# Kernel tuning notes

Measured on AMD Instinct MI355X. Metric: run time of the kernel, lower is better.

Reference implementation:

```python
import jax, jax.numpy as jnp
import numpy as np

B, S, F, H = 512, 1024, 16, 64
BN_EPS = 1e-3  # Keras BatchNormalization default epsilon


def setup_inputs() -> dict:
    key = jax.random.key(0)
    ks = jax.random.split(key, 8)
    scale = 0.1
    return {
        "inputs": jax.random.normal(ks[0], (B, S, F), dtype=jnp.float32),
        "gru_kernel": jax.random.normal(ks[1], (F - 1, 3 * H), dtype=jnp.float32) * scale,
        "gru_rec_kernel": jax.random.normal(ks[2], (H, 3 * H), dtype=jnp.float32) * scale,
        "gru_bias": jax.random.normal(ks[3], (2, 3 * H), dtype=jnp.float32) * scale,
        "w1": jax.random.normal(ks[4], (H, 64), dtype=jnp.float32) * scale,
        "b1": jnp.zeros((64,), dtype=jnp.float32),
        "bn_gamma": jnp.ones((64,), dtype=jnp.float32),
        "bn_beta": jnp.zeros((64,), dtype=jnp.float32),
        "bn_mean": jnp.zeros((64,), dtype=jnp.float32),
        "bn_var": jnp.ones((64,), dtype=jnp.float32),
        "w2": jax.random.normal(ks[5], (64, 1), dtype=jnp.float32) * scale,
        "b2": jnp.zeros((1,), dtype=jnp.float32),
        "T": jax.random.normal(ks[6], (1,), dtype=jnp.float32),
    }


def _gru_scan(x, kernel, rec_kernel, bias):
    # Keras GRU, reset_after=True, gate order (z, r, h). x: [B, S, Fin]
    b_i, b_r = bias[0], bias[1]  # input bias, recurrent bias, each [3H]
    # Precompute input projections for all timesteps: [B, S, 3H]
    x_proj = jnp.einsum("bsf,fg->bsg", x, kernel) + b_i
    h0 = jnp.zeros((x.shape[0], rec_kernel.shape[0]), dtype=x.dtype)

    def step(h, xp):
        rp = h @ rec_kernel + b_r  # [B, 3H]
        xz, xr, xh = jnp.split(xp, 3, axis=-1)
        rz, rr, rh = jnp.split(rp, 3, axis=-1)
        z = jax.nn.sigmoid(xz + rz)
        r = jax.nn.sigmoid(xr + rr)
        hh = jnp.tanh(xh + r * rh)
        h_new = z * h + (1.0 - z) * hh
        return h_new, None

    h_final, _ = jax.lax.scan(step, h0, jnp.swapaxes(x_proj, 0, 1))
    return h_final  # [B, H]


def reference(inputs, gru_kernel, gru_rec_kernel, gru_bias, w1, b1,
              bn_gamma, bn_beta, bn_mean, bn_var, w2, b2, T):
    x = inputs[:, :, :-1]                 # [B, S, F-1]
    delta_x_shifted = inputs[:, :, -1]    # [B, S]
    state = _gru_scan(x, gru_kernel, gru_rec_kernel, gru_bias)  # [B, H]
    # T * delta tiled to H then mean over time == T * mean_t(delta), broadcast over H
    delta_effect = T[0] * jnp.mean(delta_x_shifted, axis=1, keepdims=True)  # [B, 1]
    state = state + delta_effect  # broadcasts over H
    h = jax.nn.relu(state @ w1 + b1)
    # Dropout identity at inference; BatchNorm uses moving statistics
    h = (h - bn_mean) * jax.lax.rsqrt(bn_var + BN_EPS) * bn_gamma + bn_beta
    out = h @ w2 + b2  # [B, 1]
    return out
```

## Files before the change

kernel.cpp:

```cpp
#include <hip/hip_runtime.h>
#include <hip/hip_bf16.h>


#define KEEP(x) asm volatile("" : "+v"(x))

typedef _Float16 f16x2 __attribute__((ext_vector_type(2)));
union H2U { unsigned int u; f16x2 h; };
union FU  { unsigned int u; float f; };

#if defined(__has_builtin)
#  if __has_builtin(__builtin_amdgcn_fdot2)
#    define HAS_FDOT2 1
#  endif
#endif
#ifndef HAS_FDOT2
#  define HAS_FDOT2 0
#endif

static __device__ __forceinline__ float dot2acc(unsigned int hraw, unsigned int wraw, float acc) {
    H2U a, b; a.u = hraw; b.u = wraw;
#if HAS_FDOT2
    return __builtin_amdgcn_fdot2(a.h, b.h, acc, false);
#else
    return fmaf((float)a.h.x, (float)b.h.x, fmaf((float)a.h.y, (float)b.h.y, acc));
#endif
}

template<bool BF16>
struct IO {
    static __device__ __forceinline__ float ld(const void* p, int i) {
        if constexpr (BF16) {
            unsigned short u = ((const unsigned short*)p)[i];
            FU c; c.u = (unsigned int)u << 16;
            return c.f;
        } else {
            return ((const float*)p)[i];
        }
    }
    static __device__ __forceinline__ void st(void* p, int i, float v) {
        if constexpr (BF16) ((__hip_bfloat16*)p)[i] = __float2bfloat16(v);
        else ((float*)p)[i] = v;
    }
};

__global__ void detect_dtype_kernel(const void* rkbuf, int* flag) {
    const float* f = (const float*)rkbuf;
    int ok = 0;
    for (int i = 0; i < 64; ++i) {
        float a = fabsf(f[i]);
        ok += (a > 1e-5f && a < 2.0f) ? 1 : 0;
    }
    *flag = (ok >= 48) ? 1 : 0;
}

template<bool BF16>
__global__ __launch_bounds__(64, 1)
void gru_sw_kernel(const void* __restrict__ inp, const void* __restrict__ gk,
                   const void* __restrict__ rk,  const void* __restrict__ gb,
                   const void* __restrict__ w1,  const void* __restrict__ b1v,
                   const void* __restrict__ gam, const void* __restrict__ bet,
                   const void* __restrict__ muv, const void* __restrict__ vav,
                   const void* __restrict__ w2,  const void* __restrict__ bb2,
                   const void* __restrict__ Tp,  const int* __restrict__ mode,
                   void* __restrict__ out)
{
    const int want = BF16 ? 0 : 1;
    if (*mode != want) return;

    const int b = blockIdx.x;
    const int l = threadIdx.x;

    __shared__ __align__(16) unsigned char xsm[32768];
    __shared__ __align__(16) _Float16 hsf[64];
    __shared__ __align__(16) float sredf[64];

    using io = IO<BF16>;
    const uint4* gin = (const uint4*)inp;
    uint4* xv = (uint4*)xsm;

    if constexpr (BF16) {
#pragma unroll 4
        for (int i = 0; i < 32; ++i)
            xv[i*64 + l] = gin[b*2048 + i*64 + l];
    } else {
#pragma unroll 4
        for (int i = 0; i < 32; ++i)
            xv[i*64 + l] = gin[b*4096 + i*64 + l];
    }

    unsigned int wzp[32], wrp[32], whp[32];
#pragma unroll
    for (int p = 0; p < 32; ++p) {
        H2U z, r, hh;
        z.h  = f16x2{(_Float16)io::ld(rk, (2*p)*192 + l),
                     (_Float16)io::ld(rk, (2*p+1)*192 + l)};
        r.h  = f16x2{(_Float16)io::ld(rk, (2*p)*192 + 64 + l),
                     (_Float16)io::ld(rk, (2*p+1)*192 + 64 + l)};
        hh.h = f16x2{(_Float16)io::ld(rk, (2*p)*192 + 128 + l),
                     (_Float16)io::ld(rk, (2*p+1)*192 + 128 + l)};
        wzp[p] = z.u; wrp[p] = r.u; whp[p] = hh.u;
        KEEP(wzp[p]); KEEP(wrp[p]); KEEP(whp[p]);
    }
    float kzf[15], krf[15], khf[15];
#pragma unroll
    for (int c = 0; c < 15; ++c) {
        kzf[c] = io::ld(gk, c*192 + l);
        krf[c] = io::ld(gk, c*192 + 64 + l);
        khf[c] = io::ld(gk, c*192 + 128 + l);
        KEEP(kzf[c]); KEEP(krf[c]); KEEP(khf[c]);
    }
    const float bz  = io::ld(gb, l)      + io::ld(gb, 192 + l);
    const float br  = io::ld(gb, 64 + l) + io::ld(gb, 192 + 64 + l);
    const float bax = io::ld(gb, 128 + l);
    const float bah = io::ld(gb, 192 + 128 + l);

    float dsum = 0.0f;
    if constexpr (BF16) {
        const unsigned short* xs16 = (const unsigned short*)xsm;
#pragma unroll
        for (int k = 0; k < 16; ++k) {
            FU c; c.u = (unsigned int)xs16[(l + 64*k)*16 + 15] << 16;
            dsum += c.f;
        }
    } else {
        const float* xsf = (const float*)xsm;
#pragma unroll
        for (int k = 0; k < 8; ++k)
            dsum += xsf[(l + 64*k)*16 + 15];
    }

    uint4 hr[8];
#pragma unroll
    for (int i = 0; i < 8; ++i) hr[i] = make_uint4(0, 0, 0, 0);
    float h = 0.0f;

    uint4  cr16[2] = {}, pr16[2] = {};
    float4 cr32[4] = {}, pr32[4] = {};
    if constexpr (BF16) { cr16[0] = xv[0]; cr16[1] = xv[1]; }
    else { const float4* lp = (const float4*)xsm;
           cr32[0]=lp[0]; cr32[1]=lp[1]; cr32[2]=lp[2]; cr32[3]=lp[3]; }

#pragma unroll 1
    for (int s = 0; s < 1024; ++s) {
        if constexpr (!BF16) {
            if (s == 512) {
#pragma unroll 4
                for (int i = 0; i < 32; ++i)
                    xv[i*64 + l] = gin[b*4096 + 2048 + i*64 + l];
                const float* xsf = (const float*)xsm;
#pragma unroll
                for (int k = 0; k < 8; ++k)
                    dsum += xsf[(l + 64*k)*16 + 15];
                const float4* lp = (const float4*)xsm;
                cr32[0]=lp[0]; cr32[1]=lp[1]; cr32[2]=lp[2]; cr32[3]=lp[3];
            }
        }

        float xc[16];
        if constexpr (BF16) {
            const unsigned int dw[8] = {cr16[0].x, cr16[0].y, cr16[0].z, cr16[0].w,
                                        cr16[1].x, cr16[1].y, cr16[1].z, cr16[1].w};
#pragma unroll
            for (int j = 0; j < 8; ++j) {
                FU lo, hi; lo.u = dw[j] << 16; hi.u = dw[j] & 0xffff0000u;
                xc[2*j] = lo.f; xc[2*j+1] = hi.f;
            }
        } else {
            xc[0]=cr32[0].x; xc[1]=cr32[0].y; xc[2]=cr32[0].z; xc[3]=cr32[0].w;
            xc[4]=cr32[1].x; xc[5]=cr32[1].y; xc[6]=cr32[1].z; xc[7]=cr32[1].w;
            xc[8]=cr32[2].x; xc[9]=cr32[2].y; xc[10]=cr32[2].z; xc[11]=cr32[2].w;
            xc[12]=cr32[3].x; xc[13]=cr32[3].y; xc[14]=cr32[3].z; xc[15]=cr32[3].w;
        }
        float az = bz, ar_ = br, ax = bax;
#pragma unroll
        for (int c = 0; c < 15; ++c) {
            az  = fmaf(xc[c], kzf[c], az);
            ar_ = fmaf(xc[c], krf[c], ar_);
            ax  = fmaf(xc[c], khf[c], ax);
        }

        const bool pf = (s < 1023) && (BF16 || s != 511);
        if (pf) {
            if constexpr (BF16) {
                pr16[0] = xv[(s+1)*2]; pr16[1] = xv[(s+1)*2 + 1];
            } else {
                const float4* lp = (const float4*)xsm;
                pr32[0] = lp[((s+1)&511)*4];     pr32[1] = lp[((s+1)&511)*4+1];
                pr32[2] = lp[((s+1)&511)*4+2];   pr32[3] = lp[((s+1)&511)*4+3];
            }
        }

        float ah = bah;
        float az1 = 0.0f, ar1 = 0.0f, ah1 = 0.0f;
#pragma unroll
        for (int i = 0; i < 4; ++i) {
            const uint4 d = hr[i];
            az  = dot2acc(d.x, wzp[4*i+0], az);  ar_ = dot2acc(d.x, wrp[4*i+0], ar_); ah  = dot2acc(d.x, whp[4*i+0], ah);
            az  = dot2acc(d.y, wzp[4*i+1], az);  ar_ = dot2acc(d.y, wrp[4*i+1], ar_); ah  = dot2acc(d.y, whp[4*i+1], ah);
            az  = dot2acc(d.z, wzp[4*i+2], az);  ar_ = dot2acc(d.z, wrp[4*i+2], ar_); ah  = dot2acc(d.z, whp[4*i+2], ah);
            az  = dot2acc(d.w, wzp[4*i+3], az);  ar_ = dot2acc(d.w, wrp[4*i+3], ar_); ah  = dot2acc(d.w, whp[4*i+3], ah);
        }
#pragma unroll
        for (int i = 4; i < 8; ++i) {
            const uint4 d = hr[i];
            az1 = dot2acc(d.x, wzp[4*i+0], az1); ar1 = dot2acc(d.x, wrp[4*i+0], ar1); ah1 = dot2acc(d.x, whp[4*i+0], ah1);
            az1 = dot2acc(d.y, wzp[4*i+1], az1); ar1 = dot2acc(d.y, wrp[4*i+1], ar1); ah1 = dot2acc(d.y, whp[4*i+1], ah1);
            az1 = dot2acc(d.z, wzp[4*i+2], az1); ar1 = dot2acc(d.z, wrp[4*i+2], ar1); ah1 = dot2acc(d.z, whp[4*i+2], ah1);
            az1 = dot2acc(d.w, wzp[4*i+3], az1); ar1 = dot2acc(d.w, wrp[4*i+3], ar1); ah1 = dot2acc(d.w, whp[4*i+3], ah1);
        }
        az += az1; ar_ += ar1; ah += ah1;

        const float z   = __builtin_amdgcn_rcpf(1.0f + __expf(-az));
        const float r   = __builtin_amdgcn_rcpf(1.0f + __expf(-ar_));
        const float pre = fmaf(r, ah, ax);
        const float e2  = __expf(2.0f * pre);
        const float th  = 1.0f - 2.0f * __builtin_amdgcn_rcpf(e2 + 1.0f);
        h = fmaf(z, h - th, th);

        hsf[l] = (_Float16)h;
        const uint4* hp = (const uint4*)hsf;
#pragma unroll
        for (int i = 0; i < 8; ++i) hr[i] = hp[i];
        if constexpr (BF16) { cr16[0] = pr16[0]; cr16[1] = pr16[1]; }
        else { cr32[0]=pr32[0]; cr32[1]=pr32[1]; cr32[2]=pr32[2]; cr32[3]=pr32[3]; }
    }

#pragma unroll
    for (int off = 1; off < 64; off <<= 1)
        dsum += __shfl_xor(dsum, off, 64);
    const float T0 = io::ld(Tp, 0);
    const float state = fmaf(T0 * (1.0f / 1024.0f), dsum, h);
    sredf[l] = state;

    const int j = l;
    float acc = io::ld(b1v, j);
#pragma unroll
    for (int k = 0; k < 64; ++k)
        acc = fmaf(sredf[k], io::ld(w1, k*64 + j), acc);
    acc = fmaxf(acc, 0.0f);
    const float inv = rsqrtf(io::ld(vav, j) + 0.001f);
    acc = fmaf((acc - io::ld(muv, j)) * inv, io::ld(gam, j), io::ld(bet, j));

    float v = acc * io::ld(w2, j);
#pragma unroll
    for (int off = 32; off > 0; off >>= 1)
        v += __shfl_down(v, off);
    if (j == 0) io::st(out, b, v + io::ld(bb2, 0));
}

extern "C" void kernel_launch(void* const* d_in, const int* in_sizes, int n_in,
                              void* d_out, int out_size, void* d_ws, size_t ws_size,
                              hipStream_t stream)
{
    const void* inp = d_in[0];
    const void* gk  = d_in[1];
    const void* rk  = d_in[2];
    const void* gb  = d_in[3];
    const void* w1  = d_in[4];
    const void* b1v = d_in[5];
    const void* gam = d_in[6];
    const void* bet = d_in[7];
    const void* muv = d_in[8];
    const void* vav = d_in[9];
    const void* w2  = d_in[10];
    const void* bb2 = d_in[11];
    const void* Tp  = d_in[12];

    int* flag = (int*)d_ws;
    detect_dtype_kernel<<<dim3(1), dim3(1), 0, stream>>>(rk, flag);
    gru_sw_kernel<true ><<<dim3(512), dim3(64), 0, stream>>>(
        inp, gk, rk, gb, w1, b1v, gam, bet, muv, vav, w2, bb2, Tp, flag, d_out);
    gru_sw_kernel<false><<<dim3(512), dim3(64), 0, stream>>>(
        inp, gk, rk, gb, w1, b1v, gam, bet, muv, vav, w2, bb2, Tp, flag, d_out);
}
```

Baseline: 554.5 us.

## Move GRU weights from registers to LDS and overlap next-step input projection

Recurrent and input weights are no longer held in per-lane registers. They are staged into shared memory as packed uint4/float4 vectors and streamed through a software-pipelined load inside the step loop. The input projection for step s+1 is now computed after the hidden-state update of step s, which takes it off the critical path at the start of the step. This cuts register pressure but adds about 24 LDS vector loads per step to the serial recurrence. That cost can lengthen each step, since only one wave runs per block.

```diff
diff --git a/kernel.cpp b/kernel.cpp
--- a/kernel.cpp
+++ b/kernel.cpp
@@ -1,8 +1,6 @@
 #include <hip/hip_runtime.h>
 #include <hip/hip_bf16.h>
 
-
-#define KEEP(x) asm volatile("" : "+v"(x))
 
 typedef _Float16 f16x2 __attribute__((ext_vector_type(2)));
 union H2U { unsigned int u; f16x2 h; };
@@ -55,7 +53,7 @@
 
 template<bool BF16>
 __global__ __launch_bounds__(64, 1)
-void gru_sw_kernel(const void* __restrict__ inp, const void* __restrict__ gk,
+void gru_ls_kernel(const void* __restrict__ inp, const void* __restrict__ gk,
                    const void* __restrict__ rk,  const void* __restrict__ gb,
                    const void* __restrict__ w1,  const void* __restrict__ b1v,
                    const void* __restrict__ gam, const void* __restrict__ bet,
@@ -71,44 +69,55 @@
     const int l = threadIdx.x;
 
     __shared__ __align__(16) unsigned char xsm[32768];
+    __shared__ __align__(16) uint4  wvs[8*3*64];
+    __shared__ __align__(16) float4 xws[3*4*64];
     __shared__ __align__(16) _Float16 hsf[64];
     __shared__ __align__(16) float sredf[64];
 
     using io = IO<BF16>;
     const uint4* gin = (const uint4*)inp;
-    uint4* xv = (uint4*)xsm;
+    uint4* xvw = (uint4*)xsm;
 
     if constexpr (BF16) {
 #pragma unroll 4
         for (int i = 0; i < 32; ++i)
-            xv[i*64 + l] = gin[b*2048 + i*64 + l];
+            xvw[i*64 + l] = gin[b*2048 + i*64 + l];
     } else {
 #pragma unroll 4
         for (int i = 0; i < 32; ++i)
-            xv[i*64 + l] = gin[b*4096 + i*64 + l];
-    }
-
-    unsigned int wzp[32], wrp[32], whp[32];
-#pragma unroll
-    for (int p = 0; p < 32; ++p) {
-        H2U z, r, hh;
-        z.h  = f16x2{(_Float16)io::ld(rk, (2*p)*192 + l),
-                     (_Float16)io::ld(rk, (2*p+1)*192 + l)};
-        r.h  = f16x2{(_Float16)io::ld(rk, (2*p)*192 + 64 + l),
-                     (_Float16)io::ld(rk, (2*p+1)*192 + 64 + l)};
-        hh.h = f16x2{(_Float16)io::ld(rk, (2*p)*192 + 128 + l),
-                     (_Float16)io::ld(rk, (2*p+1)*192 + 128 + l)};
-        wzp[p] = z.u; wrp[p] = r.u; whp[p] = hh.u;
-        KEEP(wzp[p]); KEEP(wrp[p]); KEEP(whp[p]);
-    }
-    float kzf[15], krf[15], khf[15];
-#pragma unroll
-    for (int c = 0; c < 15; ++c) {
-        kzf[c] = io::ld(gk, c*192 + l);
-        krf[c] = io::ld(gk, c*192 + 64 + l);
-        khf[c] = io::ld(gk, c*192 + 128 + l);
-        KEEP(kzf[c]); KEEP(krf[c]); KEEP(khf[c]);
-    }
+            xvw[i*64 + l] = gin[b*4096 + i*64 + l];
+    }
+
+#pragma unroll 1
+    for (int i = 0; i < 8; ++i) {
+#pragma unroll
+        for (int g = 0; g < 3; ++g) {
+            unsigned int dw[4];
+#pragma unroll
+            for (int j = 0; j < 4; ++j) {
+                const int p = 4*i + j;
+                H2U u;
+                u.h = f16x2{(_Float16)io::ld(rk, (2*p)*192 + g*64 + l),
+                            (_Float16)io::ld(rk, (2*p+1)*192 + g*64 + l)};
+                dw[j] = u.u;
+            }
+            wvs[(i*3 + g)*64 + l] = make_uint4(dw[0], dw[1], dw[2], dw[3]);
+        }
+    }
+#pragma unroll 1
+    for (int g = 0; g < 3; ++g) {
+#pragma unroll
+        for (int j = 0; j < 4; ++j) {
+            float v[4];
+#pragma unroll
+            for (int c4 = 0; c4 < 4; ++c4) {
+                const int ch = 4*j + c4;
+                v[c4] = (ch < 15) ? io::ld(gk, ch*192 + g*64 + l) : 0.0f;
+            }
+            xws[(g*4 + j)*64 + l] = make_float4(v[0], v[1], v[2], v[3]);
+        }
+    }
+
     const float bz  = io::ld(gb, l)      + io::ld(gb, 192 + l);
     const float br  = io::ld(gb, 64 + l) + io::ld(gb, 192 + 64 + l);
     const float bax = io::ld(gb, 128 + l);
@@ -129,41 +138,24 @@
             dsum += xsf[(l + 64*k)*16 + 15];
     }
 
-    uint4 hr[8];
-#pragma unroll
-    for (int i = 0; i < 8; ++i) hr[i] = make_uint4(0, 0, 0, 0);
-    float h = 0.0f;
-
-    uint4  cr16[2] = {}, pr16[2] = {};
-    float4 cr32[4] = {}, pr32[4] = {};
-    if constexpr (BF16) { cr16[0] = xv[0]; cr16[1] = xv[1]; }
-    else { const float4* lp = (const float4*)xsm;
-           cr32[0]=lp[0]; cr32[1]=lp[1]; cr32[2]=lp[2]; cr32[3]=lp[3]; }
-
-#pragma unroll 1
-    for (int s = 0; s < 1024; ++s) {
-        if constexpr (!BF16) {
-            if (s == 512) {
-#pragma unroll 4
-                for (int i = 0; i < 32; ++i)
-                    xv[i*64 + l] = gin[b*4096 + 2048 + i*64 + l];
-                const float* xsf = (const float*)xsm;
-#pragma unroll
-                for (int k = 0; k < 8; ++k)
-                    dsum += xsf[(l + 64*k)*16 + 15];
-                const float4* lp = (const float4*)xsm;
-                cr32[0]=lp[0]; cr32[1]=lp[1]; cr32[2]=lp[2]; cr32[3]=lp[3];
-            }
-        }
-
+    const uint4*  WVl = wvs + l;
+    const float4* XWl = xws + l;
+    const uint4*  hp  = (const uint4*)hsf;
+    const uint4*  xvr = (const uint4*)xsm;
+
+    uint4  cr16[2] = {};
+    float4 cr32[4] = {};
+
+    float azc, arc, axc;
+    auto xproj = [&]() {
         float xc[16];
         if constexpr (BF16) {
             const unsigned int dw[8] = {cr16[0].x, cr16[0].y, cr16[0].z, cr16[0].w,
                                         cr16[1].x, cr16[1].y, cr16[1].z, cr16[1].w};
 #pragma unroll
-            for (int j = 0; j < 8; ++j) {
-                FU lo, hi; lo.u = dw[j] << 16; hi.u = dw[j] & 0xffff0000u;
-                xc[2*j] = lo.f; xc[2*j+1] = hi.f;
+            for (int j2 = 0; j2 < 8; ++j2) {
+                FU lo, hi; lo.u = dw[j2] << 16; hi.u = dw[j2] & 0xffff0000u;
+                xc[2*j2] = lo.f; xc[2*j2+1] = hi.f;
             }
         } else {
             xc[0]=cr32[0].x; xc[1]=cr32[0].y; xc[2]=cr32[0].z; xc[3]=cr32[0].w;
@@ -171,42 +163,88 @@
             xc[8]=cr32[2].x; xc[9]=cr32[2].y; xc[10]=cr32[2].z; xc[11]=cr32[2].w;
             xc[12]=cr32[3].x; xc[13]=cr32[3].y; xc[14]=cr32[3].z; xc[15]=cr32[3].w;
         }
+        const float4 qz0 = XWl[0],   qz1 = XWl[64],  qz2 = XWl[128], qz3 = XWl[192];
+        const float4 qr0 = XWl[256], qr1 = XWl[320], qr2 = XWl[384], qr3 = XWl[448];
+        const float4 qh0 = XWl[512], qh1 = XWl[576], qh2 = XWl[640], qh3 = XWl[704];
         float az = bz, ar_ = br, ax = bax;
-#pragma unroll
-        for (int c = 0; c < 15; ++c) {
-            az  = fmaf(xc[c], kzf[c], az);
-            ar_ = fmaf(xc[c], krf[c], ar_);
-            ax  = fmaf(xc[c], khf[c], ax);
-        }
-
-        const bool pf = (s < 1023) && (BF16 || s != 511);
-        if (pf) {
+        az=fmaf(xc[0],qz0.x,az);  ar_=fmaf(xc[0],qr0.x,ar_);  ax=fmaf(xc[0],qh0.x,ax);
+        az=fmaf(xc[1],qz0.y,az);  ar_=fmaf(xc[1],qr0.y,ar_);  ax=fmaf(xc[1],qh0.y,ax);
+        az=fmaf(xc[2],qz0.z,az);  ar_=fmaf(xc[2],qr0.z,ar_);  ax=fmaf(xc[2],qh0.z,ax);
+        az=fmaf(xc[3],qz0.w,az);  ar_=fmaf(xc[3],qr0.w,ar_);  ax=fmaf(xc[3],qh0.w,ax);
+        az=fmaf(xc[4],qz1.x,az);  ar_=fmaf(xc[4],qr1.x,ar_);  ax=fmaf(xc[4],qh1.x,ax);
+        az=fmaf(xc[5],qz1.y,az);  ar_=fmaf(xc[5],qr1.y,ar_);  ax=fmaf(xc[5],qh1.y,ax);
+        az=fmaf(xc[6],qz1.z,az);  ar_=fmaf(xc[6],qr1.z,ar_);  ax=fmaf(xc[6],qh1.z,ax);
+        az=fmaf(xc[7],qz1.w,az);  ar_=fmaf(xc[7],qr1.w,ar_);  ax=fmaf(xc[7],qh1.w,ax);
+        az=fmaf(xc[8],qz2.x,az);  ar_=fmaf(xc[8],qr2.x,ar_);  ax=fmaf(xc[8],qh2.x,ax);
+        az=fmaf(xc[9],qz2.y,az);  ar_=fmaf(xc[9],qr2.y,ar_);  ax=fmaf(xc[9],qh2.y,ax);
+        az=fmaf(xc[10],qz2.z,az); ar_=fmaf(xc[10],qr2.z,ar_); ax=fmaf(xc[10],qh2.z,ax);
+        az=fmaf(xc[11],qz2.w,az); ar_=fmaf(xc[11],qr2.w,ar_); ax=fmaf(xc[11],qh2.w,ax);
+        az=fmaf(xc[12],qz3.x,az); ar_=fmaf(xc[12],qr3.x,ar_); ax=fmaf(xc[12],qh3.x,ax);
+        az=fmaf(xc[13],qz3.y,az); ar_=fmaf(xc[13],qr3.y,ar_); ax=fmaf(xc[13],qh3.y,ax);
+        az=fmaf(xc[14],qz3.z,az); ar_=fmaf(xc[14],qr3.z,ar_); ax=fmaf(xc[14],qh3.z,ax);
+        az=fmaf(xc[15],qz3.w,az); ar_=fmaf(xc[15],qr3.w,ar_); ax=fmaf(xc[15],qh3.w,ax);
+        azc = az; arc = ar_; axc = ax;
+    };
+
+    if constexpr (BF16) { cr16[0] = xvr[0]; cr16[1] = xvr[1]; }
+    else { const float4* lp = (const float4*)xsm;
+           cr32[0]=lp[0]; cr32[1]=lp[1]; cr32[2]=lp[2]; cr32[3]=lp[3]; }
+    xproj();
+
+    uint4 hr[8];
+#pragma unroll
+    for (int i = 0; i < 8; ++i) hr[i] = make_uint4(0, 0, 0, 0);
+    float h = 0.0f;
+
+#pragma unroll 1
+    for (int s = 0; s < 1024; ++s) {
+        if constexpr (!BF16) {
+            if (s == 511) {
+#pragma unroll 4
+                for (int i = 0; i < 32; ++i)
+                    xvw[i*64 + l] = gin[b*4096 + 2048 + i*64 + l];
+                const float* xsf = (const float*)xsm;
+#pragma unroll
+                for (int k = 0; k < 8; ++k)
+                    dsum += xsf[(l + 64*k)*16 + 15];
+            }
+        }
+        if (s < 1023) {
             if constexpr (BF16) {
-                pr16[0] = xv[(s+1)*2]; pr16[1] = xv[(s+1)*2 + 1];
+                cr16[0] = xvr[(s+1)*2]; cr16[1] = xvr[(s+1)*2 + 1];
             } else {
                 const float4* lp = (const float4*)xsm;
-                pr32[0] = lp[((s+1)&511)*4];     pr32[1] = lp[((s+1)&511)*4+1];
-                pr32[2] = lp[((s+1)&511)*4+2];   pr32[3] = lp[((s+1)&511)*4+3];
-            }
-        }
-
+                const int ix = ((s+1) & 511) * 4;
+                cr32[0]=lp[ix]; cr32[1]=lp[ix+1]; cr32[2]=lp[ix+2]; cr32[3]=lp[ix+3];
+            }
+        }
+
+        float az = azc, ar_ = arc;
+        const float ax = axc;
         float ah = bah;
         float az1 = 0.0f, ar1 = 0.0f, ah1 = 0.0f;
-#pragma unroll
-        for (int i = 0; i < 4; ++i) {
+        uint4 cz = WVl[0], crr = WVl[64], chh = WVl[128];
+#pragma unroll
+        for (int i = 0; i < 8; ++i) {
+            uint4 nz, nr, nh;
+            if (i < 7) {
+                nz = WVl[(i+1)*192];
+                nr = WVl[(i+1)*192 + 64];
+                nh = WVl[(i+1)*192 + 128];
+            }
             const uint4 d = hr[i];
-            az  = dot2acc(d.x, wzp[4*i+0], az);  ar_ = dot2acc(d.x, wrp[4*i+0], ar_); ah  = dot2acc(d.x, whp[4*i+0], ah);
-            az  = dot2acc(d.y, wzp[4*i+1], az);  ar_ = dot2acc(d.y, wrp[4*i+1], ar_); ah  = dot2acc(d.y, whp[4*i+1], ah);
-            az  = dot2acc(d.z, wzp[4*i+2], az);  ar_ = dot2acc(d.z, wrp[4*i+2], ar_); ah  = dot2acc(d.z, whp[4*i+2], ah);
-            az  = dot2acc(d.w, wzp[4*i+3], az);  ar_ = dot2acc(d.w, wrp[4*i+3], ar_); ah  = dot2acc(d.w, whp[4*i+3], ah);
-        }
-#pragma unroll
-        for (int i = 4; i < 8; ++i) {
-            const uint4 d = hr[i];
-            az1 = dot2acc(d.x, wzp[4*i+0], az1); ar1 = dot2acc(d.x, wrp[4*i+0], ar1); ah1 = dot2acc(d.x, whp[4*i+0], ah1);
-            az1 = dot2acc(d.y, wzp[4*i+1], az1); ar1 = dot2acc(d.y, wrp[4*i+1], ar1); ah1 = dot2acc(d.y, whp[4*i+1], ah1);
-            az1 = dot2acc(d.z, wzp[4*i+2], az1); ar1 = dot2acc(d.z, wrp[4*i+2], ar1); ah1 = dot2acc(d.z, whp[4*i+2], ah1);
-            az1 = dot2acc(d.w, wzp[4*i+3], az1); ar1 = dot2acc(d.w, wrp[4*i+3], ar1); ah1 = dot2acc(d.w, whp[4*i+3], ah1);
+            if (i < 4) {
+                az  = dot2acc(d.x, cz.x, az);  ar_ = dot2acc(d.x, crr.x, ar_); ah  = dot2acc(d.x, chh.x, ah);
+                az  = dot2acc(d.y, cz.y, az);  ar_ = dot2acc(d.y, crr.y, ar_); ah  = dot2acc(d.y, chh.y, ah);
+                az  = dot2acc(d.z, cz.z, az);  ar_ = dot2acc(d.z, crr.z, ar_); ah  = dot2acc(d.z, chh.z, ah);
+                az  = dot2acc(d.w, cz.w, az);  ar_ = dot2acc(d.w, crr.w, ar_); ah  = dot2acc(d.w, chh.w, ah);
+            } else {
+                az1 = dot2acc(d.x, cz.x, az1); ar1 = dot2acc(d.x, crr.x, ar1); ah1 = dot2acc(d.x, chh.x, ah1);
+                az1 = dot2acc(d.y, cz.y, az1); ar1 = dot2acc(d.y, crr.y, ar1); ah1 = dot2acc(d.y, chh.y, ah1);
+                az1 = dot2acc(d.z, cz.z, az1); ar1 = dot2acc(d.z, crr.z, ar1); ah1 = dot2acc(d.z, chh.z, ah1);
+                az1 = dot2acc(d.w, cz.w, az1); ar1 = dot2acc(d.w, crr.w, ar1); ah1 = dot2acc(d.w, chh.w, ah1);
+            }
+            cz = nz; crr = nr; chh = nh;
         }
         az += az1; ar_ += ar1; ah += ah1;
 
@@ -218,11 +256,10 @@
         h = fmaf(z, h - th, th);
 
         hsf[l] = (_Float16)h;
-        const uint4* hp = (const uint4*)hsf;
 #pragma unroll
         for (int i = 0; i < 8; ++i) hr[i] = hp[i];
-        if constexpr (BF16) { cr16[0] = pr16[0]; cr16[1] = pr16[1]; }
-        else { cr32[0]=pr32[0]; cr32[1]=pr32[1]; cr32[2]=pr32[2]; cr32[3]=pr32[3]; }
+
+        if (s < 1023) xproj();
     }
 
 #pragma unroll
@@ -268,8 +305,8 @@
 
     int* flag = (int*)d_ws;
     detect_dtype_kernel<<<dim3(1), dim3(1), 0, stream>>>(rk, flag);
-    gru_sw_kernel<true ><<<dim3(512), dim3(64), 0, stream>>>(
+    gru_ls_kernel<true ><<<dim3(512), dim3(64), 0, stream>>>(
         inp, gk, rk, gb, w1, b1v, gam, bet, muv, vav, w2, bb2, Tp, flag, d_out);
-    gru_sw_kernel<false><<<dim3(512), dim3(64), 0, stream>>>(
+    gru_ls_kernel<false><<<dim3(512), dim3(64), 0, stream>>>(
         inp, gk, rk, gb, w1, b1v, gam, bet, muv, vav, w2, bb2, Tp, flag, d_out);
 }
```

After: 508.5 us. 1.09x faster.

## Pack input projection to fp16 dot2 with LDS-staged weights and split gate chains

Applied to the files above, without the earlier changes.

Replaces the per-step fp32 FMA input projection with packed fp16 dot2 operations. The input-kernel weights are staged in LDS as packed halves and reloaded each step, which frees about 45 VGPRs of fp32 weights. The recurrent matvec is reordered so z is computed first, then r, then h, letting the sigmoid transcendentals overlap the later dot chains. The fp32 second-half refill moves to step 511 and the next-x prefetch moves after the h computation, at the cost of fp16 rounding of the inputs and their weights.

```diff
diff --git a/kernel.cpp b/kernel.cpp
--- a/kernel.cpp
+++ b/kernel.cpp
@@ -17,13 +17,20 @@
 #  define HAS_FDOT2 0
 #endif
 
-static __device__ __forceinline__ float dot2acc(unsigned int hraw, unsigned int wraw, float acc) {
-    H2U a, b; a.u = hraw; b.u = wraw;
+static __device__ __forceinline__ float dot2acc(unsigned int araw, unsigned int braw, float acc) {
+    H2U a, b; a.u = araw; b.u = braw;
 #if HAS_FDOT2
     return __builtin_amdgcn_fdot2(a.h, b.h, acc, false);
 #else
     return fmaf((float)a.h.x, (float)b.h.x, fmaf((float)a.h.y, (float)b.h.y, acc));
 #endif
+}
+
+static __device__ __forceinline__ unsigned int pk16(float lo, float hi) {
+    auto v = __builtin_amdgcn_cvt_pkrtz(lo, hi);
+    union { decltype(v) h; unsigned int u; } u;
+    u.h = v;
+    return u.u;
 }
 
 template<bool BF16>
@@ -55,7 +62,7 @@
 
 template<bool BF16>
 __global__ __launch_bounds__(64, 1)
-void gru_sw_kernel(const void* __restrict__ inp, const void* __restrict__ gk,
+void gru_sx_kernel(const void* __restrict__ inp, const void* __restrict__ gk,
                    const void* __restrict__ rk,  const void* __restrict__ gb,
                    const void* __restrict__ w1,  const void* __restrict__ b1v,
                    const void* __restrict__ gam, const void* __restrict__ bet,
@@ -71,21 +78,39 @@
     const int l = threadIdx.x;
 
     __shared__ __align__(16) unsigned char xsm[32768];
+    __shared__ __align__(16) uint4 xws4[6*64];
     __shared__ __align__(16) _Float16 hsf[64];
     __shared__ __align__(16) float sredf[64];
 
     using io = IO<BF16>;
     const uint4* gin = (const uint4*)inp;
-    uint4* xv = (uint4*)xsm;
+    uint4* xvw = (uint4*)xsm;
 
     if constexpr (BF16) {
 #pragma unroll 4
         for (int i = 0; i < 32; ++i)
-            xv[i*64 + l] = gin[b*2048 + i*64 + l];
+            xvw[i*64 + l] = gin[b*2048 + i*64 + l];
     } else {
 #pragma unroll 4
         for (int i = 0; i < 32; ++i)
-            xv[i*64 + l] = gin[b*4096 + i*64 + l];
+            xvw[i*64 + l] = gin[b*4096 + i*64 + l];
+    }
+
+#pragma unroll 1
+    for (int g = 0; g < 3; ++g) {
+#pragma unroll
+        for (int q = 0; q < 2; ++q) {
+            unsigned int d[4];
+#pragma unroll
+            for (int j = 0; j < 4; ++j) {
+                const int pj = q*4 + j;
+                const int c0 = 2*pj, c1 = 2*pj + 1;
+                const float f0 = (c0 < 15) ? io::ld(gk, c0*192 + g*64 + l) : 0.0f;
+                const float f1 = (c1 < 15) ? io::ld(gk, c1*192 + g*64 + l) : 0.0f;
+                d[j] = pk16(f0, f1);
+            }
+            xws4[(g*2 + q)*64 + l] = make_uint4(d[0], d[1], d[2], d[3]);
+        }
     }
 
     unsigned int wzp[32], wrp[32], whp[32];
@@ -101,14 +126,6 @@
         wzp[p] = z.u; wrp[p] = r.u; whp[p] = hh.u;
         KEEP(wzp[p]); KEEP(wrp[p]); KEEP(whp[p]);
     }
-    float kzf[15], krf[15], khf[15];
-#pragma unroll
-    for (int c = 0; c < 15; ++c) {
-        kzf[c] = io::ld(gk, c*192 + l);
-        krf[c] = io::ld(gk, c*192 + 64 + l);
-        khf[c] = io::ld(gk, c*192 + 128 + l);
-        KEEP(kzf[c]); KEEP(krf[c]); KEEP(khf[c]);
-    }
     const float bz  = io::ld(gb, l)      + io::ld(gb, 192 + l);
     const float br  = io::ld(gb, 64 + l) + io::ld(gb, 192 + 64 + l);
     const float bax = io::ld(gb, 128 + l);
@@ -129,98 +146,158 @@
             dsum += xsf[(l + 64*k)*16 + 15];
     }
 
+    const uint4* hp  = (const uint4*)hsf;
+    const uint4* xvr = (const uint4*)xsm;
+
+    uint4  cr16[2] = {}, pr16[2] = {};
+    float4 cr32[4] = {}, pr32[4] = {};
+    if constexpr (BF16) { cr16[0] = xvr[0]; cr16[1] = xvr[1]; }
+    else { const float4* lp = (const float4*)xsm;
+           cr32[0]=lp[0]; cr32[1]=lp[1]; cr32[2]=lp[2]; cr32[3]=lp[3]; }
+
+    uint4 xwq0, xwq1, xwq2, xwq3, xwq4, xwq5;
+    {
+        const uint4* xq = xws4 + l;
+        xwq0 = xq[0];   xwq1 = xq[64];  xwq2 = xq[128];
+        xwq3 = xq[192]; xwq4 = xq[256]; xwq5 = xq[320];
+    }
+
     uint4 hr[8];
 #pragma unroll
     for (int i = 0; i < 8; ++i) hr[i] = make_uint4(0, 0, 0, 0);
     float h = 0.0f;
-
-    uint4  cr16[2] = {}, pr16[2] = {};
-    float4 cr32[4] = {}, pr32[4] = {};
-    if constexpr (BF16) { cr16[0] = xv[0]; cr16[1] = xv[1]; }
-    else { const float4* lp = (const float4*)xsm;
-           cr32[0]=lp[0]; cr32[1]=lp[1]; cr32[2]=lp[2]; cr32[3]=lp[3]; }
 
 #pragma unroll 1
     for (int s = 0; s < 1024; ++s) {
         if constexpr (!BF16) {
-            if (s == 512) {
+            if (s == 511) {
 #pragma unroll 4
                 for (int i = 0; i < 32; ++i)
-                    xv[i*64 + l] = gin[b*4096 + 2048 + i*64 + l];
+                    xvw[i*64 + l] = gin[b*4096 + 2048 + i*64 + l];
                 const float* xsf = (const float*)xsm;
 #pragma unroll
                 for (int k = 0; k < 8; ++k)
                     dsum += xsf[(l + 64*k)*16 + 15];
-                const float4* lp = (const float4*)xsm;
-                cr32[0]=lp[0]; cr32[1]=lp[1]; cr32[2]=lp[2]; cr32[3]=lp[3];
             }
         }
 
-        float xc[16];
+        unsigned int xcp[8];
         if constexpr (BF16) {
             const unsigned int dw[8] = {cr16[0].x, cr16[0].y, cr16[0].z, cr16[0].w,
                                         cr16[1].x, cr16[1].y, cr16[1].z, cr16[1].w};
 #pragma unroll
             for (int j = 0; j < 8; ++j) {
                 FU lo, hi; lo.u = dw[j] << 16; hi.u = dw[j] & 0xffff0000u;
-                xc[2*j] = lo.f; xc[2*j+1] = hi.f;
+                xcp[j] = pk16(lo.f, hi.f);
             }
         } else {
-            xc[0]=cr32[0].x; xc[1]=cr32[0].y; xc[2]=cr32[0].z; xc[3]=cr32[0].w;
-            xc[4]=cr32[1].x; xc[5]=cr32[1].y; xc[6]=cr32[1].z; xc[7]=cr32[1].w;
-            xc[8]=cr32[2].x; xc[9]=cr32[2].y; xc[10]=cr32[2].z; xc[11]=cr32[2].w;
-            xc[12]=cr32[3].x; xc[13]=cr32[3].y; xc[14]=cr32[3].z; xc[15]=cr32[3].w;
-        }
-        float az = bz, ar_ = br, ax = bax;
-#pragma unroll
-        for (int c = 0; c < 15; ++c) {
-            az  = fmaf(xc[c], kzf[c], az);
-            ar_ = fmaf(xc[c], krf[c], ar_);
-            ax  = fmaf(xc[c], khf[c], ax);
-        }
-
-        const bool pf = (s < 1023) && (BF16 || s != 511);
-        if (pf) {
-            if constexpr (BF16) {
-                pr16[0] = xv[(s+1)*2]; pr16[1] = xv[(s+1)*2 + 1];
-            } else {
-                const float4* lp = (const float4*)xsm;
-                pr32[0] = lp[((s+1)&511)*4];     pr32[1] = lp[((s+1)&511)*4+1];
-                pr32[2] = lp[((s+1)&511)*4+2];   pr32[3] = lp[((s+1)&511)*4+3];
-            }
-        }
-
-        float ah = bah;
-        float az1 = 0.0f, ar1 = 0.0f, ah1 = 0.0f;
+            const float xf[16] = {cr32[0].x,cr32[0].y,cr32[0].z,cr32[0].w,
+                                  cr32[1].x,cr32[1].y,cr32[1].z,cr32[1].w,
+                                  cr32[2].x,cr32[2].y,cr32[2].z,cr32[2].w,
+                                  cr32[3].x,cr32[3].y,cr32[3].z,cr32[3].w};
+#pragma unroll
+            for (int j = 0; j < 8; ++j) xcp[j] = pk16(xf[2*j], xf[2*j+1]);
+        }
+
+        float az = bz, arr = br, ax = bax;
+        {
+            const unsigned int wzx[8] = {xwq0.x,xwq0.y,xwq0.z,xwq0.w, xwq1.x,xwq1.y,xwq1.z,xwq1.w};
+            const unsigned int wrx[8] = {xwq2.x,xwq2.y,xwq2.z,xwq2.w, xwq3.x,xwq3.y,xwq3.z,xwq3.w};
+            const unsigned int whx[8] = {xwq4.x,xwq4.y,xwq4.z,xwq4.w, xwq5.x,xwq5.y,xwq5.z,xwq5.w};
+#pragma unroll
+            for (int j = 0; j < 8; ++j) az  = dot2acc(xcp[j], wzx[j], az);
+#pragma unroll
+            for (int j = 0; j < 8; ++j) arr = dot2acc(xcp[j], wrx[j], arr);
+#pragma unroll
+            for (int j = 0; j < 8; ++j) ax  = dot2acc(xcp[j], whx[j], ax);
+        }
+
+        {
+            unsigned int zz;
+            asm volatile("s_mov_b32 %0, 0" : "=s"(zz));
+            const uint4* xq = xws4 + l + zz;
+            xwq0 = xq[0];   xwq1 = xq[64];  xwq2 = xq[128];
+            xwq3 = xq[192]; xwq4 = xq[256]; xwq5 = xq[320];
+        }
+
+        float az1 = 0.0f;
 #pragma unroll
         for (int i = 0; i < 4; ++i) {
             const uint4 d = hr[i];
-            az  = dot2acc(d.x, wzp[4*i+0], az);  ar_ = dot2acc(d.x, wrp[4*i+0], ar_); ah  = dot2acc(d.x, whp[4*i+0], ah);
-            az  = dot2acc(d.y, wzp[4*i+1], az);  ar_ = dot2acc(d.y, wrp[4*i+1], ar_); ah  = dot2acc(d.y, whp[4*i+1], ah);
-            az  = dot2acc(d.z, wzp[4*i+2], az);  ar_ = dot2acc(d.z, wrp[4*i+2], ar_); ah  = dot2acc(d.z, whp[4*i+2], ah);
-            az  = dot2acc(d.w, wzp[4*i+3], az);  ar_ = dot2acc(d.w, wrp[4*i+3], ar_); ah  = dot2acc(d.w, whp[4*i+3], ah);
+            az  = dot2acc(d.x, wzp[4*i+0], az);
+            az  = dot2acc(d.y, wzp[4*i+1], az);
+            az  = dot2acc(d.z, wzp[4*i+2], az);
+            az  = dot2acc(d.w, wzp[4*i+3], az);
         }
 #pragma unroll
         for (int i = 4; i < 8; ++i) {
             const uint4 d = hr[i];
-            az1 = dot2acc(d.x, wzp[4*i+0], az1); ar1 = dot2acc(d.x, wrp[4*i+0], ar1); ah1 = dot2acc(d.x, whp[4*i+0], ah1);
-            az1 = dot2acc(d.y, wzp[4*i+1], az1); ar1 = dot2acc(d.y, wrp[4*i+1], ar1); ah1 = dot2acc(d.y, whp[4*i+1], ah1);
-            az1 = dot2acc(d.z, wzp[4*i+2], az1); ar1 = dot2acc(d.z, wrp[4*i+2], ar1); ah1 = dot2acc(d.z, whp[4*i+2], ah1);
-            az1 = dot2acc(d.w, wzp[4*i+3], az1); ar1 = dot2acc(d.w, wrp[4*i+3], ar1); ah1 = dot2acc(d.w, whp[4*i+3], ah1);
-        }
-        az += az1; ar_ += ar1; ah += ah1;
-
-        const float z   = __builtin_amdgcn_rcpf(1.0f + __expf(-az));
-        const float r   = __builtin_amdgcn_rcpf(1.0f + __expf(-ar_));
+            az1 = dot2acc(d.x, wzp[4*i+0], az1);
+            az1 = dot2acc(d.y, wzp[4*i+1], az1);
+            az1 = dot2acc(d.z, wzp[4*i+2], az1);
+            az1 = dot2acc(d.w, wzp[4*i+3], az1);
+        }
+        az += az1;
+        const float z = __builtin_amdgcn_rcpf(1.0f + __expf(-az));
+
+        float ar1 = 0.0f;
+#pragma unroll
+        for (int i = 0; i < 4; ++i) {
+            const uint4 d = hr[i];
+            arr = dot2acc(d.x, wrp[4*i+0], arr);
+            arr = dot2acc(d.y, wrp[4*i+1], arr);
+            arr = dot2acc(d.z, wrp[4*i+2], arr);
+            arr = dot2acc(d.w, wrp[4*i+3], arr);
+        }
+#pragma unroll
+        for (int i = 4; i < 8; ++i) {
+            const uint4 d = hr[i];
+            ar1 = dot2acc(d.x, wrp[4*i+0], ar1);
+            ar1 = dot2acc(d.y, wrp[4*i+1], ar1);
+            ar1 = dot2acc(d.z, wrp[4*i+2], ar1);
+            ar1 = dot2acc(d.w, wrp[4*i+3], ar1);
+        }
+        arr += ar1;
+        const float r = __builtin_amdgcn_rcpf(1.0f + __expf(-arr));
+
+        float ah = bah, ah1 = 0.0f;
+#pragma unroll
+        for (int i = 0; i < 4; ++i) {
+            const uint4 d = hr[i];
+            ah  = dot2acc(d.x, whp[4*i+0], ah);
+            ah  = dot2acc(d.y, whp[4*i+1], ah);
+            ah  = dot2acc(d.z, whp[4*i+2], ah);
+            ah  = dot2acc(d.w, whp[4*i+3], ah);
+        }
+#pragma unroll
+        for (int i = 4; i < 8; ++i) {
+            const uint4 d = hr[i];
+            ah1 = dot2acc(d.x, whp[4*i+0], ah1);
+            ah1 = dot2acc(d.y, whp[4*i+1], ah1);
+            ah1 = dot2acc(d.z, whp[4*i+2], ah1);
+            ah1 = dot2acc(d.w, whp[4*i+3], ah1);
+        }
+        ah += ah1;
+
         const float pre = fmaf(r, ah, ax);
         const float e2  = __expf(2.0f * pre);
         const float th  = 1.0f - 2.0f * __builtin_amdgcn_rcpf(e2 + 1.0f);
         h = fmaf(z, h - th, th);
 
+        if (s < 1023) {
+            if constexpr (BF16) {
+                pr16[0] = xvr[(s+1)*2]; pr16[1] = xvr[(s+1)*2 + 1];
+            } else {
+                const float4* lp = (const float4*)xsm;
+                const int ix = ((s+1) & 511) * 4;
+                pr32[0]=lp[ix]; pr32[1]=lp[ix+1]; pr32[2]=lp[ix+2]; pr32[3]=lp[ix+3];
+            }
+        }
+
         hsf[l] = (_Float16)h;
-        const uint4* hp = (const uint4*)hsf;
 #pragma unroll
         for (int i = 0; i < 8; ++i) hr[i] = hp[i];
+
         if constexpr (BF16) { cr16[0] = pr16[0]; cr16[1] = pr16[1]; }
         else { cr32[0]=pr32[0]; cr32[1]=pr32[1]; cr32[2]=pr32[2]; cr32[3]=pr32[3]; }
     }
@@ -268,8 +345,8 @@
 
     int* flag = (int*)d_ws;
     detect_dtype_kernel<<<dim3(1), dim3(1), 0, stream>>>(rk, flag);
-    gru_sw_kernel<true ><<<dim3(512), dim3(64), 0, stream>>>(
+    gru_sx_kernel<true ><<<dim3(512), dim3(64), 0, stream>>>(
         inp, gk, rk, gb, w1, b1v, gam, bet, muv, vav, w2, bb2, Tp, flag, d_out);
-    gru_sw_kernel<false><<<dim3(512), dim3(64), 0, stream>>>(
+    gru_sx_kernel<false><<<dim3(512), dim3(64), 0, stream>>>(
         inp, gk, rk, gb, w1, b1v, gam, bet, muv, vav, w2, bb2, Tp, flag, d_out);
 }
```

After: 577.1 us. +4.1%, slower.
